# Kernel optimization log

Hardware: AMD Instinct MI355X
Metric: run time of the kernel (lower is better)

Reference implementation:

```python
import jax, jax.numpy as jnp
import numpy as np
from jax import lax

DIM = 256
NUM_HEADS = 8
HEAD_DIM = DIM // NUM_HEADS          # 32
KEY_DIM = int(HEAD_DIM * 0.5)        # 16
SCALE = KEY_DIM ** -0.5
H_QKV = DIM + KEY_DIM * NUM_HEADS * 2  # 512
BN_EPS = 1e-3  # keras BatchNormalization default epsilon


def conv_bn(x, w, gamma, beta, mean, var, groups=1):
    # Conv2D (no bias) + BatchNorm (inference), activation=None
    y = lax.conv_general_dilated(
        x, w, window_strides=(1, 1), padding='SAME',
        dimension_numbers=('NHWC', 'HWIO', 'NHWC'),
        feature_group_count=groups)
    return gamma * (y - mean) * lax.rsqrt(var + BN_EPS) + beta


def setup_inputs() -> dict:
    key = jax.random.key(0)
    ks = jax.random.split(key, 4)
    B, Hs, Ws = 8, 32, 32
    inp = {
        'inputs': jax.random.normal(ks[0], (B, Hs, Ws, DIM), dtype=jnp.float32),
        # qkv: 1x1 conv dim -> h
        'qkv_w': jax.random.normal(ks[1], (1, 1, DIM, H_QKV), dtype=jnp.float32) * 0.05,
        'qkv_gamma': jnp.ones((H_QKV,), jnp.float32),
        'qkv_beta': jnp.zeros((H_QKV,), jnp.float32),
        'qkv_mean': jnp.zeros((H_QKV,), jnp.float32),
        'qkv_var': jnp.ones((H_QKV,), jnp.float32),
        # pe: 3x3 depthwise conv (groups=dim)
        'pe_w': jax.random.normal(ks[2], (3, 3, 1, DIM), dtype=jnp.float32) * 0.05,
        'pe_gamma': jnp.ones((DIM,), jnp.float32),
        'pe_beta': jnp.zeros((DIM,), jnp.float32),
        'pe_mean': jnp.zeros((DIM,), jnp.float32),
        'pe_var': jnp.ones((DIM,), jnp.float32),
        # proj: 1x1 conv dim -> dim
        'proj_w': jax.random.normal(ks[3], (1, 1, DIM, DIM), dtype=jnp.float32) * 0.05,
        'proj_gamma': jnp.ones((DIM,), jnp.float32),
        'proj_beta': jnp.zeros((DIM,), jnp.float32),
        'proj_mean': jnp.zeros((DIM,), jnp.float32),
        'proj_var': jnp.ones((DIM,), jnp.float32),
    }
    return inp


def reference(inputs, qkv_w, qkv_gamma, qkv_beta, qkv_mean, qkv_var,
              pe_w, pe_gamma, pe_beta, pe_mean, pe_var,
              proj_w, proj_gamma, proj_beta, proj_mean, proj_var):
    B, Hs, Ws, C = inputs.shape
    N = Hs * Ws
    x = conv_bn(inputs, qkv_w, qkv_gamma, qkv_beta, qkv_mean, qkv_var)  # [B,H,W,h]
    x = x.reshape(B, N, NUM_HEADS, 2 * KEY_DIM + HEAD_DIM)
    q = x[..., :KEY_DIM]                          # [B,N,nh,kd]
    k = x[..., KEY_DIM:2 * KEY_DIM]               # [B,N,nh,kd]
    v = x[..., 2 * KEY_DIM:]                      # [B,N,nh,hd]
    # attn = q^T @ k^T : [B,nh,N,N]
    attn = jnp.einsum('bnhk,bmhk->bhnm', q, k) * SCALE
    attn = jax.nn.softmax(attn, axis=-1)
    # x = v^T @ attn : [B,nh,hd,N]
    x = jnp.einsum('bnhd,bhnm->bhdm', v, attn)
    # faithful to source: transpose [0,2,1,3] -> [B,hd,nh,N], then reshape NHWC
    x = jnp.transpose(x, (0, 2, 1, 3)).reshape(B, Hs, Ws, C)
    pe = conv_bn(v.reshape(B, Hs, Ws, C), pe_w, pe_gamma, pe_beta, pe_mean, pe_var, groups=C)
    x = x + pe
    x = conv_bn(x, proj_w, proj_gamma, proj_beta, proj_mean, proj_var)
    return x
```

## Files before the change

kernel.cpp:

```cpp
#include <hip/hip_runtime.h>

typedef _Float16 h4 __attribute__((ext_vector_type(4)));
typedef _Float16 h8 __attribute__((ext_vector_type(8)));
typedef float    f4 __attribute__((ext_vector_type(4)));

#define QSCALE (0.25f * 1.44269504088896f)

__device__ __forceinline__ float ex2(float x){ return __builtin_amdgcn_exp2f(x); }

__global__ __launch_bounds__(256) void prep_k(
    const float* __restrict__ X,
    const float* __restrict__ qkvw, const float* __restrict__ qg, const float* __restrict__ qb,
    const float* __restrict__ qm,   const float* __restrict__ qv,
    const float* __restrict__ pew,  const float* __restrict__ pg, const float* __restrict__ pb,
    const float* __restrict__ pm,   const float* __restrict__ pv,
    const float* __restrict__ prw,  const float* __restrict__ prg, const float* __restrict__ prb,
    const float* __restrict__ prm,  const float* __restrict__ prv,
    _Float16* __restrict__ Xh, _Float16* __restrict__ Wqkv, float* __restrict__ bqkv,
    _Float16* __restrict__ Wproj, float* __restrict__ bproj,
    float* __restrict__ peW, float* __restrict__ peB)
{
  const int gid = blockIdx.x*256 + threadIdx.x;
  const int gsz = gridDim.x*256;
  for (int i = gid; i < 2097152/4; i += gsz){
    const float4 xv = ((const float4*)X)[i];
    h4 o; o[0]=(_Float16)xv.x; o[1]=(_Float16)xv.y; o[2]=(_Float16)xv.z; o[3]=(_Float16)xv.w;
    ((h4*)Xh)[i] = o;
  }
  for (int i = gid; i < 512*256; i += gsz){
    int o = i >> 8, c = i & 255;
    float s = qg[o] * rsqrtf(qv[o] + 1e-3f);
    Wqkv[i] = (_Float16)(qkvw[c*512 + o] * s);
  }
  for (int i = gid; i < 512; i += gsz){
    float s = qg[i] * rsqrtf(qv[i] + 1e-3f);
    bqkv[i] = qb[i] - qm[i]*s;
  }
  for (int i = gid; i < 256*256; i += gsz){
    int o = i >> 8, c = i & 255;
    float s = prg[o] * rsqrtf(prv[o] + 1e-3f);
    Wproj[i] = (_Float16)(prw[c*256 + o] * s);
  }
  for (int i = gid; i < 256; i += gsz){
    float s = prg[i] * rsqrtf(prv[i] + 1e-3f);
    bproj[i] = prb[i] - prm[i]*s;
  }
  for (int i = gid; i < 9*256; i += gsz){
    int c = i & 255;
    float s = pg[c] * rsqrtf(pv[c] + 1e-3f);
    peW[i] = pew[i] * s;
  }
  for (int i = gid; i < 256; i += gsz){
    float s = pg[i] * rsqrtf(pv[i] + 1e-3f);
    peB[i] = pb[i] - pm[i]*s;
  }
}

template<int EPI, int MT>
__global__ __launch_bounds__(256) void gemm_k(
    const _Float16* __restrict__ A, const _Float16* __restrict__ Bt,
    const float* __restrict__ bias,
    _Float16* __restrict__ Qh, _Float16* __restrict__ Kh, _Float16* __restrict__ Vh,
    float* __restrict__ Out)
{
  const int t = threadIdx.x, lane = t & 63, wv = t >> 6;
  const int l15 = lane & 15, q = lane >> 4;
  const int mb = (blockIdx.x*4 + wv) * (16*MT);
  const int n0 = blockIdx.y * 64;
  f4 acc[MT][4] = {};
  #pragma unroll
  for (int kk = 0; kk < 8; ++kk){
    h8 af[MT];
    #pragma unroll
    for (int mi = 0; mi < MT; ++mi)
      af[mi] = *(const h8*)(A + (size_t)(mb + mi*16 + l15)*256 + kk*32 + q*8);
    #pragma unroll
    for (int nj = 0; nj < 4; ++nj){
      h8 bf = *(const h8*)(Bt + (size_t)(n0 + nj*16 + l15)*256 + kk*32 + q*8);
      #pragma unroll
      for (int mi = 0; mi < MT; ++mi)
        acc[mi][nj] = __builtin_amdgcn_mfma_f32_16x16x32_f16(af[mi], bf, acc[mi][nj], 0,0,0);
    }
  }
  #pragma unroll
  for (int mi = 0; mi < MT; ++mi)
  #pragma unroll
  for (int nj = 0; nj < 4; ++nj){
    const int og = n0 + nj*16 + l15;
    const float bs = bias[og];
    #pragma unroll
    for (int r = 0; r < 4; ++r){
      const int mg = mb + mi*16 + q*4 + r;
      const float v = acc[mi][nj][r] + bs;
      if (EPI == 0){
        const int h = og >> 6, j = og & 63;
        const int b = mg >> 10, n = mg & 1023;
        const size_t bhn = (size_t)(b*8+h)*1024 + n;
        if (j < 16)      Qh[bhn*16 + j]      = (_Float16)(v * QSCALE);
        else if (j < 32) Kh[bhn*16 + (j-16)] = (_Float16)v;
        else             Vh[bhn*32 + (j-32)] = (_Float16)v;
      } else {
        Out[(size_t)mg*256 + og] = v;
      }
    }
  }
}

__global__ __launch_bounds__(256) void pass1_k(
    const _Float16* __restrict__ Qh, const _Float16* __restrict__ Kh,
    const _Float16* __restrict__ Vh, _Float16* __restrict__ Vs)
{
  const int t = threadIdx.x, lane = t & 63, wv = t >> 6;
  const int l15 = lane & 15, q = lane >> 4;
  const int bh = blockIdx.y;
  const int n0 = (blockIdx.x*4 + wv) * 32;
  const size_t qb = (size_t)bh*1024;
  const h4 af0 = *(const h4*)(Qh + (qb + n0 + l15)*16 + q*4);
  const h4 af1 = *(const h4*)(Qh + (qb + n0 + 16 + l15)*16 + q*4);
  f4 sm0 = {0.f,0.f,0.f,0.f}, sm1 = {0.f,0.f,0.f,0.f};
  const _Float16* kp = Kh + qb*16;
  #pragma unroll 4
  for (int mt = 0; mt < 64; ++mt){
    h4 bf = *(const h4*)(kp + mt*256 + l15*16 + q*4);
    f4 z = {0.f,0.f,0.f,0.f};
    f4 d0 = __builtin_amdgcn_mfma_f32_16x16x16f16(af0, bf, z, 0,0,0);
    f4 d1 = __builtin_amdgcn_mfma_f32_16x16x16f16(af1, bf, z, 0,0,0);
    #pragma unroll
    for (int r = 0; r < 4; ++r){ sm0[r] += ex2(d0[r]); sm1[r] += ex2(d1[r]); }
  }
  #pragma unroll
  for (int st = 1; st < 16; st <<= 1){
    #pragma unroll
    for (int r = 0; r < 4; ++r){
      sm0[r] += __shfl_xor(sm0[r], st, 64);
      sm1[r] += __shfl_xor(sm1[r], st, 64);
    }
  }
  f4 cv0, cv1;
  #pragma unroll
  for (int r = 0; r < 4; ++r){ cv0[r] = 1.0f/sm0[r]; cv1[r] = 1.0f/sm1[r]; }
  #pragma unroll
  for (int half = 0; half < 2; ++half){
    const int dd = l15 + half*16;
    h4 o0, o1;
    #pragma unroll
    for (int r = 0; r < 4; ++r){
      o0[r] = (_Float16)((float)Vh[(qb + n0 + q*4 + r)*32 + dd] * cv0[r]);
      o1[r] = (_Float16)((float)Vh[(qb + n0 + 16 + q*4 + r)*32 + dd] * cv1[r]);
    }
    *(h4*)(Vs + ((size_t)bh*32 + dd)*1024 + n0 + q*4)      = o0;
    *(h4*)(Vs + ((size_t)bh*32 + dd)*1024 + n0 + 16 + q*4) = o1;
  }
}

__global__ __launch_bounds__(256) void pass2_k(
    const _Float16* __restrict__ Qh, const _Float16* __restrict__ Kh,
    const _Float16* __restrict__ Vs, _Float16* __restrict__ X1h)
{
  __shared__ float Tt[4][32*33];
  const int t = threadIdx.x, lane = t & 63, wv = t >> 6;
  const int l15 = lane & 15, q = lane >> 4;
  const int bh = blockIdx.y;
  const int b  = bh >> 3, h = bh & 7;
  const int mb = (blockIdx.x*4 + wv) * 32;
  const size_t qb = (size_t)bh*1024;
  const h4 kf0 = *(const h4*)(Kh + (qb + mb + l15)*16 + q*4);
  const h4 kf1 = *(const h4*)(Kh + (qb + mb + 16 + l15)*16 + q*4);
  const _Float16* qp  = Qh + qb*16;
  const _Float16* vp0 = Vs + ((size_t)bh*32 + l15)*1024;
  const _Float16* vp1 = vp0 + 16*1024;
  f4 a00={0.f,0.f,0.f,0.f}, a01={0.f,0.f,0.f,0.f};
  f4 a10={0.f,0.f,0.f,0.f}, a11={0.f,0.f,0.f,0.f};
  #pragma unroll 2
  for (int nt = 0; nt < 1024; nt += 16){
    h4 qf = *(const h4*)(qp + (nt + l15)*16 + q*4);
    h4 b0 = *(const h4*)(vp0 + nt + q*4);
    h4 b1 = *(const h4*)(vp1 + nt + q*4);
    f4 z = {0.f,0.f,0.f,0.f};
    f4 s0 = __builtin_amdgcn_mfma_f32_16x16x16f16(qf, kf0, z, 0,0,0);
    f4 s1 = __builtin_amdgcn_mfma_f32_16x16x16f16(qf, kf1, z, 0,0,0);
    h4 p0, p1;
    #pragma unroll
    for (int r = 0; r < 4; ++r){ p0[r] = (_Float16)ex2(s0[r]); p1[r] = (_Float16)ex2(s1[r]); }
    a00 = __builtin_amdgcn_mfma_f32_16x16x16f16(p0, b0, a00, 0,0,0);
    a01 = __builtin_amdgcn_mfma_f32_16x16x16f16(p0, b1, a01, 0,0,0);
    a10 = __builtin_amdgcn_mfma_f32_16x16x16f16(p1, b0, a10, 0,0,0);
    a11 = __builtin_amdgcn_mfma_f32_16x16x16f16(p1, b1, a11, 0,0,0);
  }
  #pragma unroll
  for (int r = 0; r < 4; ++r){
    Tt[wv][(q*4 + r)*33      + l15]      = a00[r];
    Tt[wv][(q*4 + r)*33      + 16 + l15] = a01[r];
    Tt[wv][(16 + q*4 + r)*33 + l15]      = a10[r];
    Tt[wv][(16 + q*4 + r)*33 + 16 + l15] = a11[r];
  }
  __syncthreads();
  _Float16* xb = X1h + (size_t)b*262144 + (size_t)h*1024 + mb;
  const int mloc = lane & 31, dh = lane >> 5;
  #pragma unroll
  for (int r = 0; r < 16; ++r){
    const int d = r*2 + dh;
    xb[(size_t)d*8192 + mloc] = (_Float16)Tt[wv][mloc*33 + d];
  }
}

__global__ __launch_bounds__(256) void pe_add_k(
    const _Float16* __restrict__ Vh, const _Float16* __restrict__ X1h,
    const float* __restrict__ peW, const float* __restrict__ peB,
    _Float16* __restrict__ X2h)
{
  const int idx = blockIdx.x*256 + threadIdx.x;
  const int c = idx & 255;
  const int tok = idx >> 8;
  const int b = tok >> 10, n = tok & 1023;
  const int hs = n >> 5, ws = n & 31;
  const int h = c >> 5, d = c & 31;
  float acc = peB[c];
  const _Float16* vb = Vh + (size_t)(b*8 + h)*32768 + d;
  #pragma unroll
  for (int dy = 0; dy < 3; ++dy){
    const int y = hs + dy - 1;
    if ((unsigned)y < 32u){
      #pragma unroll
      for (int dx = 0; dx < 3; ++dx){
        const int x = ws + dx - 1;
        if ((unsigned)x < 32u)
          acc += peW[(dy*3+dx)*256 + c] * (float)vb[(size_t)(y*32 + x)*32];
      }
    }
  }
  X2h[idx] = (_Float16)((float)X1h[idx] + acc);
}

extern "C" void kernel_launch(void* const* d_in, const int* in_sizes, int n_in,
                              void* d_out, int out_size, void* d_ws, size_t ws_size,
                              hipStream_t stream)
{
  const float* X    = (const float*)d_in[0];
  const float* qkvw = (const float*)d_in[1];
  const float* qg   = (const float*)d_in[2];
  const float* qb   = (const float*)d_in[3];
  const float* qm   = (const float*)d_in[4];
  const float* qv   = (const float*)d_in[5];
  const float* pew  = (const float*)d_in[6];
  const float* pg   = (const float*)d_in[7];
  const float* pb   = (const float*)d_in[8];
  const float* pm   = (const float*)d_in[9];
  const float* pv   = (const float*)d_in[10];
  const float* prw  = (const float*)d_in[11];
  const float* prg  = (const float*)d_in[12];
  const float* prb  = (const float*)d_in[13];
  const float* prm  = (const float*)d_in[14];
  const float* prv  = (const float*)d_in[15];

  char* ws = (char*)d_ws;
  _Float16* Xh    = (_Float16*)(ws + 0);
  _Float16* X2h   = (_Float16*)(ws + 0);
  _Float16* Qh    = (_Float16*)(ws + 4194304);
  _Float16* Kh    = (_Float16*)(ws + 6291456);
  _Float16* Vh    = (_Float16*)(ws + 8388608);
  _Float16* Vs    = (_Float16*)(ws + 12582912);
  _Float16* X1h   = (_Float16*)(ws + 16777216);
  _Float16* Wqkv  = (_Float16*)(ws + 20971520);
  float*    bqkv  = (float*)   (ws + 21233664);
  _Float16* Wproj = (_Float16*)(ws + 21235712);
  float*    bproj = (float*)   (ws + 21366784);
  float*    peW   = (float*)   (ws + 21367808);
  float*    peB   = (float*)   (ws + 21377024);

  prep_k<<<256, 256, 0, stream>>>(X, qkvw, qg, qb, qm, qv, pew, pg, pb, pm, pv,
                                  prw, prg, prb, prm, prv,
                                  Xh, Wqkv, bqkv, Wproj, bproj, peW, peB);
  gemm_k<0,2><<<dim3(64, 8), 256, 0, stream>>>(Xh, Wqkv, bqkv, Qh, Kh, Vh, nullptr);
  pass1_k<<<dim3(8, 64), 256, 0, stream>>>(Qh, Kh, Vh, Vs);
  pass2_k<<<dim3(8, 64), 256, 0, stream>>>(Qh, Kh, Vs, X1h);
  pe_add_k<<<8192, 256, 0, stream>>>(Vh, X1h, peW, peB, X2h);
  gemm_k<1,1><<<dim3(128, 4), 256, 0, stream>>>(X2h, Wproj, bproj,
                                                nullptr, nullptr, nullptr, (float*)d_out);
}
```

Baseline: 181.8 us.

## Stage GEMM and attention operands through shared memory and vectorize pe_add

Both GEMMs now load A/B tiles cooperatively into padded LDS with register prefetch of the next k-slice, and four waves share one tile in a 2x2 layout. Pass1 and pass2 stage K, Q and V chunks of 64 tokens in LDS, so the waves of a block share those loads instead of each re-reading them from global memory. pe_add processes eight channels per thread with vector loads, and prep_k launches with more blocks. The changes cut redundant global traffic at the cost of extra barriers and LDS use.

```diff
diff --git a/kernel.cpp b/kernel.cpp
--- a/kernel.cpp
+++ b/kernel.cpp
@@ -57,40 +57,60 @@
 }
 
 template<int EPI, int MT>
-__global__ __launch_bounds__(256) void gemm_k(
+__global__ __launch_bounds__(256) void gemm_staged_k(
     const _Float16* __restrict__ A, const _Float16* __restrict__ Bt,
     const float* __restrict__ bias,
     _Float16* __restrict__ Qh, _Float16* __restrict__ Kh, _Float16* __restrict__ Vh,
     float* __restrict__ Out)
 {
+  constexpr int BM = MT*32;
+  constexpr int AR = BM/64;
+  __shared__ __align__(16) _Float16 As[BM*40];
+  __shared__ __align__(16) _Float16 Bs[64*40];
   const int t = threadIdx.x, lane = t & 63, wv = t >> 6;
   const int l15 = lane & 15, q = lane >> 4;
-  const int mb = (blockIdx.x*4 + wv) * (16*MT);
-  const int n0 = blockIdx.y * 64;
-  f4 acc[MT][4] = {};
+  const int wr = wv & 1, wc = wv >> 1;
+  const int m0 = blockIdx.x*BM, n0 = blockIdx.y*64;
+  const int r4 = t >> 2, s4 = t & 3;
+  uint4 ar[AR], br;
+  #pragma unroll
+  for (int i = 0; i < AR; ++i)
+    ar[i] = *(const uint4*)(A + (size_t)(m0 + r4 + i*64)*256 + s4*8);
+  br = *(const uint4*)(Bt + (size_t)(n0 + r4)*256 + s4*8);
+  f4 acc[MT][2] = {};
   #pragma unroll
   for (int kk = 0; kk < 8; ++kk){
-    h8 af[MT];
-    #pragma unroll
-    for (int mi = 0; mi < MT; ++mi)
-      af[mi] = *(const h8*)(A + (size_t)(mb + mi*16 + l15)*256 + kk*32 + q*8);
-    #pragma unroll
-    for (int nj = 0; nj < 4; ++nj){
-      h8 bf = *(const h8*)(Bt + (size_t)(n0 + nj*16 + l15)*256 + kk*32 + q*8);
-      #pragma unroll
-      for (int mi = 0; mi < MT; ++mi)
-        acc[mi][nj] = __builtin_amdgcn_mfma_f32_16x16x32_f16(af[mi], bf, acc[mi][nj], 0,0,0);
-    }
+    #pragma unroll
+    for (int i = 0; i < AR; ++i)
+      *(uint4*)&As[(r4 + i*64)*40 + s4*8] = ar[i];
+    *(uint4*)&Bs[r4*40 + s4*8] = br;
+    __syncthreads();
+    if (kk < 7){
+      #pragma unroll
+      for (int i = 0; i < AR; ++i)
+        ar[i] = *(const uint4*)(A + (size_t)(m0 + r4 + i*64)*256 + (kk+1)*32 + s4*8);
+      br = *(const uint4*)(Bt + (size_t)(n0 + r4)*256 + (kk+1)*32 + s4*8);
+    }
+    #pragma unroll
+    for (int mi = 0; mi < MT; ++mi){
+      h8 af = *(const h8*)&As[(wr*(MT*16) + mi*16 + l15)*40 + q*8];
+      #pragma unroll
+      for (int nj = 0; nj < 2; ++nj){
+        h8 bf = *(const h8*)&Bs[(wc*32 + nj*16 + l15)*40 + q*8];
+        acc[mi][nj] = __builtin_amdgcn_mfma_f32_16x16x32_f16(af, bf, acc[mi][nj], 0,0,0);
+      }
+    }
+    __syncthreads();
   }
   #pragma unroll
   for (int mi = 0; mi < MT; ++mi)
   #pragma unroll
-  for (int nj = 0; nj < 4; ++nj){
-    const int og = n0 + nj*16 + l15;
+  for (int nj = 0; nj < 2; ++nj){
+    const int og = n0 + wc*32 + nj*16 + l15;
     const float bs = bias[og];
     #pragma unroll
     for (int r = 0; r < 4; ++r){
-      const int mg = mb + mi*16 + q*4 + r;
+      const int mg = m0 + wr*(MT*16) + mi*16 + q*4 + r;
       const float v = acc[mi][nj][r] + bs;
       if (EPI == 0){
         const int h = og >> 6, j = og & 63;
@@ -110,6 +130,7 @@
     const _Float16* __restrict__ Qh, const _Float16* __restrict__ Kh,
     const _Float16* __restrict__ Vh, _Float16* __restrict__ Vs)
 {
+  __shared__ __align__(16) _Float16 Ks[64*24];
   const int t = threadIdx.x, lane = t & 63, wv = t >> 6;
   const int l15 = lane & 15, q = lane >> 4;
   const int bh = blockIdx.y;
@@ -119,14 +140,24 @@
   const h4 af1 = *(const h4*)(Qh + (qb + n0 + 16 + l15)*16 + q*4);
   f4 sm0 = {0.f,0.f,0.f,0.f}, sm1 = {0.f,0.f,0.f,0.f};
   const _Float16* kp = Kh + qb*16;
-  #pragma unroll 4
-  for (int mt = 0; mt < 64; ++mt){
-    h4 bf = *(const h4*)(kp + mt*256 + l15*16 + q*4);
-    f4 z = {0.f,0.f,0.f,0.f};
-    f4 d0 = __builtin_amdgcn_mfma_f32_16x16x16f16(af0, bf, z, 0,0,0);
-    f4 d1 = __builtin_amdgcn_mfma_f32_16x16x16f16(af1, bf, z, 0,0,0);
-    #pragma unroll
-    for (int r = 0; r < 4; ++r){ sm0[r] += ex2(d0[r]); sm1[r] += ex2(d1[r]); }
+  const int sr = t >> 1, ss = t & 1;
+  uint4 kr;
+  if (t < 128) kr = *(const uint4*)(kp + sr*16 + ss*8);
+  for (int mt = 0; mt < 1024; mt += 64){
+    if (t < 128) *(uint4*)&Ks[sr*24 + ss*8] = kr;
+    __syncthreads();
+    if (t < 128 && mt + 64 < 1024)
+      kr = *(const uint4*)(kp + (mt + 64 + sr)*16 + ss*8);
+    #pragma unroll
+    for (int sub = 0; sub < 4; ++sub){
+      h4 bf = *(const h4*)&Ks[(sub*16 + l15)*24 + q*4];
+      f4 z = {0.f,0.f,0.f,0.f};
+      f4 d0 = __builtin_amdgcn_mfma_f32_16x16x16f16(af0, bf, z, 0,0,0);
+      f4 d1 = __builtin_amdgcn_mfma_f32_16x16x16f16(af1, bf, z, 0,0,0);
+      #pragma unroll
+      for (int r = 0; r < 4; ++r){ sm0[r] += ex2(d0[r]); sm1[r] += ex2(d1[r]); }
+    }
+    __syncthreads();
   }
   #pragma unroll
   for (int st = 1; st < 16; st <<= 1){
@@ -157,6 +188,8 @@
     const _Float16* __restrict__ Qh, const _Float16* __restrict__ Kh,
     const _Float16* __restrict__ Vs, _Float16* __restrict__ X1h)
 {
+  __shared__ __align__(16) _Float16 Qs[64*24];
+  __shared__ __align__(16) _Float16 Vss[32*72];
   __shared__ float Tt[4][32*33];
   const int t = threadIdx.x, lane = t & 63, wv = t >> 6;
   const int l15 = lane & 15, q = lane >> 4;
@@ -166,26 +199,40 @@
   const size_t qb = (size_t)bh*1024;
   const h4 kf0 = *(const h4*)(Kh + (qb + mb + l15)*16 + q*4);
   const h4 kf1 = *(const h4*)(Kh + (qb + mb + 16 + l15)*16 + q*4);
-  const _Float16* qp  = Qh + qb*16;
-  const _Float16* vp0 = Vs + ((size_t)bh*32 + l15)*1024;
-  const _Float16* vp1 = vp0 + 16*1024;
+  const _Float16* qp = Qh + qb*16;
+  const _Float16* vp = Vs + (size_t)bh*32*1024;
+  const int sr = t >> 1, ss = t & 1;
+  const int vd = t >> 3, vc = (t & 7)*8;
+  uint4 qr, vr;
+  if (t < 128) qr = *(const uint4*)(qp + sr*16 + ss*8);
+  vr = *(const uint4*)(vp + (size_t)vd*1024 + vc);
   f4 a00={0.f,0.f,0.f,0.f}, a01={0.f,0.f,0.f,0.f};
   f4 a10={0.f,0.f,0.f,0.f}, a11={0.f,0.f,0.f,0.f};
-  #pragma unroll 2
-  for (int nt = 0; nt < 1024; nt += 16){
-    h4 qf = *(const h4*)(qp + (nt + l15)*16 + q*4);
-    h4 b0 = *(const h4*)(vp0 + nt + q*4);
-    h4 b1 = *(const h4*)(vp1 + nt + q*4);
-    f4 z = {0.f,0.f,0.f,0.f};
-    f4 s0 = __builtin_amdgcn_mfma_f32_16x16x16f16(qf, kf0, z, 0,0,0);
-    f4 s1 = __builtin_amdgcn_mfma_f32_16x16x16f16(qf, kf1, z, 0,0,0);
-    h4 p0, p1;
-    #pragma unroll
-    for (int r = 0; r < 4; ++r){ p0[r] = (_Float16)ex2(s0[r]); p1[r] = (_Float16)ex2(s1[r]); }
-    a00 = __builtin_amdgcn_mfma_f32_16x16x16f16(p0, b0, a00, 0,0,0);
-    a01 = __builtin_amdgcn_mfma_f32_16x16x16f16(p0, b1, a01, 0,0,0);
-    a10 = __builtin_amdgcn_mfma_f32_16x16x16f16(p1, b0, a10, 0,0,0);
-    a11 = __builtin_amdgcn_mfma_f32_16x16x16f16(p1, b1, a11, 0,0,0);
+  for (int nt = 0; nt < 1024; nt += 64){
+    if (t < 128) *(uint4*)&Qs[sr*24 + ss*8] = qr;
+    *(uint4*)&Vss[vd*72 + vc] = vr;
+    __syncthreads();
+    if (nt + 64 < 1024){
+      if (t < 128) qr = *(const uint4*)(qp + (nt + 64 + sr)*16 + ss*8);
+      vr = *(const uint4*)(vp + (size_t)vd*1024 + nt + 64 + vc);
+    }
+    #pragma unroll
+    for (int sub = 0; sub < 4; ++sub){
+      h4 qf = *(const h4*)&Qs[(sub*16 + l15)*24 + q*4];
+      h4 b0 = *(const h4*)&Vss[l15*72      + sub*16 + q*4];
+      h4 b1 = *(const h4*)&Vss[(16+l15)*72 + sub*16 + q*4];
+      f4 z = {0.f,0.f,0.f,0.f};
+      f4 s0 = __builtin_amdgcn_mfma_f32_16x16x16f16(qf, kf0, z, 0,0,0);
+      f4 s1 = __builtin_amdgcn_mfma_f32_16x16x16f16(qf, kf1, z, 0,0,0);
+      h4 p0, p1;
+      #pragma unroll
+      for (int r = 0; r < 4; ++r){ p0[r] = (_Float16)ex2(s0[r]); p1[r] = (_Float16)ex2(s1[r]); }
+      a00 = __builtin_amdgcn_mfma_f32_16x16x16f16(p0, b0, a00, 0,0,0);
+      a01 = __builtin_amdgcn_mfma_f32_16x16x16f16(p0, b1, a01, 0,0,0);
+      a10 = __builtin_amdgcn_mfma_f32_16x16x16f16(p1, b0, a10, 0,0,0);
+      a11 = __builtin_amdgcn_mfma_f32_16x16x16f16(p1, b1, a11, 0,0,0);
+    }
+    __syncthreads();
   }
   #pragma unroll
   for (int r = 0; r < 4; ++r){
@@ -209,14 +256,20 @@
     const float* __restrict__ peW, const float* __restrict__ peB,
     _Float16* __restrict__ X2h)
 {
-  const int idx = blockIdx.x*256 + threadIdx.x;
-  const int c = idx & 255;
-  const int tok = idx >> 8;
+  const int u = blockIdx.x*256 + threadIdx.x;
+  const int c0 = (u & 31) * 8;
+  const int tok = u >> 5;
   const int b = tok >> 10, n = tok & 1023;
   const int hs = n >> 5, ws = n & 31;
-  const int h = c >> 5, d = c & 31;
-  float acc = peB[c];
-  const _Float16* vb = Vh + (size_t)(b*8 + h)*32768 + d;
+  const int h = c0 >> 5, d0 = c0 & 31;
+  const size_t idx8 = (size_t)tok*256 + c0;
+  float acc[8];
+  {
+    f4 b0v = *(const f4*)(peB + c0), b1v = *(const f4*)(peB + c0 + 4);
+    #pragma unroll
+    for (int j = 0; j < 4; ++j){ acc[j] = b0v[j]; acc[4+j] = b1v[j]; }
+  }
+  const _Float16* vb = Vh + (size_t)(b*8 + h)*32768 + d0;
   #pragma unroll
   for (int dy = 0; dy < 3; ++dy){
     const int y = hs + dy - 1;
@@ -224,12 +277,25 @@
       #pragma unroll
       for (int dx = 0; dx < 3; ++dx){
         const int x = ws + dx - 1;
-        if ((unsigned)x < 32u)
-          acc += peW[(dy*3+dx)*256 + c] * (float)vb[(size_t)(y*32 + x)*32];
+        if ((unsigned)x < 32u){
+          const int kk = dy*3 + dx;
+          h8 vv = *(const h8*)(vb + (size_t)(y*32 + x)*32);
+          f4 w0 = *(const f4*)(peW + kk*256 + c0);
+          f4 w1 = *(const f4*)(peW + kk*256 + c0 + 4);
+          #pragma unroll
+          for (int j = 0; j < 4; ++j){
+            acc[j]   += w0[j] * (float)vv[j];
+            acc[4+j] += w1[j] * (float)vv[4+j];
+          }
+        }
       }
     }
   }
-  X2h[idx] = (_Float16)((float)X1h[idx] + acc);
+  h8 x1 = *(const h8*)(X1h + idx8);
+  h8 o;
+  #pragma unroll
+  for (int j = 0; j < 8; ++j) o[j] = (_Float16)((float)x1[j] + acc[j]);
+  *(h8*)(X2h + idx8) = o;
 }
 
 extern "C" void kernel_launch(void* const* d_in, const int* in_sizes, int n_in,
@@ -268,13 +334,15 @@
   float*    peW   = (float*)   (ws + 21367808);
   float*    peB   = (float*)   (ws + 21377024);
 
-  prep_k<<<256, 256, 0, stream>>>(X, qkvw, qg, qb, qm, qv, pew, pg, pb, pm, pv,
+  prep_k<<<512, 256, 0, stream>>>(X, qkvw, qg, qb, qm, qv, pew, pg, pb, pm, pv,
                                   prw, prg, prb, prm, prv,
                                   Xh, Wqkv, bqkv, Wproj, bproj, peW, peB);
-  gemm_k<0,2><<<dim3(64, 8), 256, 0, stream>>>(Xh, Wqkv, bqkv, Qh, Kh, Vh, nullptr);
+  gemm_staged_k<0,4><<<dim3(64, 8), 256, 0, stream>>>(Xh, Wqkv, bqkv,
+                                                      Qh, Kh, Vh, nullptr);
   pass1_k<<<dim3(8, 64), 256, 0, stream>>>(Qh, Kh, Vh, Vs);
   pass2_k<<<dim3(8, 64), 256, 0, stream>>>(Qh, Kh, Vs, X1h);
-  pe_add_k<<<8192, 256, 0, stream>>>(Vh, X1h, peW, peB, X2h);
-  gemm_k<1,1><<<dim3(128, 4), 256, 0, stream>>>(X2h, Wproj, bproj,
-                                                nullptr, nullptr, nullptr, (float*)d_out);
-}
+  pe_add_k<<<1024, 256, 0, stream>>>(Vh, X1h, peW, peB, X2h);
+  gemm_staged_k<1,2><<<dim3(128, 4), 256, 0, stream>>>(X2h, Wproj, bproj,
+                                                       nullptr, nullptr, nullptr,
+                                                       (float*)d_out);
+}
```

After: 150.8 us. -17.1%, faster.
